# Kernel tuning notes

Hardware: AMD Instinct MI355X
Metric: run time of the kernel (lower is better)

## Reference

```python
import jax, jax.numpy as jnp
import numpy as np

B, S, D, H = 2, 2048, 1024, 16
DH = D // H  # 64


def setup_inputs() -> dict:
    key = jax.random.key(0)
    ks = jax.random.split(key, 12)
    std = 1.0 / np.sqrt(D)
    inp = {
        "query": jax.random.normal(ks[0], (B, S, D), jnp.float32),
        "key": jax.random.normal(ks[1], (B, S, D), jnp.float32),
        "value": jax.random.normal(ks[2], (B, S, D), jnp.float32),
        # causal mask: 1.0 where attention is disallowed (j > i)
        "mask": jnp.triu(jnp.ones((S, S), jnp.float32), k=1)[None, None, :, :] * jnp.ones((B, 1, 1, 1), jnp.float32),
        "Wq": jax.random.normal(ks[3], (D, D), jnp.float32) * std,
        "bq": jnp.zeros((D,), jnp.float32),
        "Wk": jax.random.normal(ks[4], (D, D), jnp.float32) * std,
        "bk": jnp.zeros((D,), jnp.float32),
        "Wv": jax.random.normal(ks[5], (D, D), jnp.float32) * std,
        "bv": jnp.zeros((D,), jnp.float32),
        "Wo": jax.random.normal(ks[6], (D, D), jnp.float32) * std,
        "bo": jnp.zeros((D,), jnp.float32),
    }
    return inp


def _split_heads(x):
    b, s, _ = x.shape
    return x.reshape(b, s, H, DH).transpose(0, 2, 1, 3)  # [B,H,S,DH]


def reference(query, key, value, mask, Wq, bq, Wk, bk, Wv, bv, Wo, bo):
    q = _split_heads(query @ Wq + bq)
    k = _split_heads(key @ Wk + bk)
    v = _split_heads(value @ Wv + bv)
    scale = jnp.sqrt(jnp.asarray(DH, jnp.float32))
    scores = jnp.einsum("bhqd,bhkd->bhqk", q, k) / scale
    scores = scores + mask * (-1e9)
    attn = jax.nn.softmax(scores, axis=-1)  # [B,H,S,S]
    out = jnp.einsum("bhqk,bhkd->bhqd", attn, v)
    out = out.transpose(0, 2, 1, 3).reshape(query.shape[0], -1, D)
    out = out @ Wo + bo
    return (out, attn)
```

## Files before the change

kernel.cpp:

```cpp
#include <hip/hip_runtime.h>
#include <hip/hip_bf16.h>

typedef __bf16 bf16;
typedef __bf16 bf16x8 __attribute__((ext_vector_type(8)));
typedef __bf16 bf16x4 __attribute__((ext_vector_type(4)));
typedef float f32x4 __attribute__((ext_vector_type(4)));

#define S_LEN 2048
#define D_MODEL 1024
#define N_HEADS 16
#define D_HEAD 64
#define M_ROWS 4096

__global__ void cvt_f32_bf16(const float* __restrict__ in, bf16* __restrict__ out, int n) {
    int i = (blockIdx.x * blockDim.x + threadIdx.x) * 4;
    int stride = gridDim.x * blockDim.x * 4;
    for (; i < n; i += stride) {
        f32x4 v = *(const f32x4*)(in + i);
        bf16x4 o;
        o[0] = (bf16)v[0]; o[1] = (bf16)v[1]; o[2] = (bf16)v[2]; o[3] = (bf16)v[3];
        *(bf16x4*)(out + i) = o;
    }
}

__global__ void cvtT_f32_bf16(const float* __restrict__ in, bf16* __restrict__ out) {
    __shared__ float t[32][33];
    int k0 = blockIdx.x * 32, n0 = blockIdx.y * 32;
    int lr = threadIdx.x & 31, lc = threadIdx.x >> 5;
#pragma unroll
    for (int p = 0; p < 4; ++p)
        t[lc + p * 8][lr] = in[(size_t)(k0 + lc + p * 8) * D_MODEL + n0 + lr];
    __syncthreads();
#pragma unroll
    for (int p = 0; p < 4; ++p)
        out[(size_t)(n0 + lc + p * 8) * D_MODEL + k0 + lr] = (bf16)t[lr][lc + p * 8];
}

__global__ __launch_bounds__(256) void gemm_bf16(
    const bf16* __restrict__ A, const bf16* __restrict__ Bt,
    const float* __restrict__ bias, bf16* __restrict__ outh,
    float* __restrict__ outf, int mode) {
    const int K = D_MODEL;
    __shared__ bf16 Als[128][80];
    __shared__ bf16 Bls[128][80];
    const int tid = threadIdx.x;
    const int lane = tid & 63, wave = tid >> 6;
    const int wm = wave >> 1, wn = wave & 1;
    const int g = lane >> 4, r16 = lane & 15;
    const int m0 = blockIdx.x * 128, n0 = blockIdx.y * 128;
    const int srow = tid >> 3, scol = (tid & 7) * 8;
    f32x4 acc[4][4] = {};
    for (int kt = 0; kt < K; kt += 64) {
        __syncthreads();
#pragma unroll
        for (int p = 0; p < 4; ++p) {
            int row = p * 32 + srow;
            *(bf16x8*)&Als[row][scol] = *(const bf16x8*)(A + (size_t)(m0 + row) * K + kt + scol);
            *(bf16x8*)&Bls[row][scol] = *(const bf16x8*)(Bt + (size_t)(n0 + row) * K + kt + scol);
        }
        __syncthreads();
#pragma unroll
        for (int kk = 0; kk < 2; ++kk) {
            bf16x8 af[4], bfr[4];
#pragma unroll
            for (int i = 0; i < 4; ++i) af[i] = *(const bf16x8*)&Als[wm * 64 + i * 16 + r16][kk * 32 + g * 8];
#pragma unroll
            for (int j = 0; j < 4; ++j) bfr[j] = *(const bf16x8*)&Bls[wn * 64 + j * 16 + r16][kk * 32 + g * 8];
#pragma unroll
            for (int i = 0; i < 4; ++i)
#pragma unroll
                for (int j = 0; j < 4; ++j)
                    acc[i][j] = __builtin_amdgcn_mfma_f32_16x16x32_bf16(af[i], bfr[j], acc[i][j], 0, 0, 0);
        }
    }
#pragma unroll
    for (int i = 0; i < 4; ++i) {
#pragma unroll
        for (int j = 0; j < 4; ++j) {
            int col = n0 + wn * 64 + j * 16 + r16;
            float bv = bias[col];
#pragma unroll
            for (int r = 0; r < 4; ++r) {
                int row = m0 + wm * 64 + i * 16 + g * 4 + r;
                float v = acc[i][j][r] + bv;
                if (mode == 0) {
                    int b = row >> 11, s = row & (S_LEN - 1);
                    int h = col >> 6, dh = col & 63;
                    outh[(size_t)(((b * N_HEADS + h) * S_LEN) + s) * D_HEAD + dh] = (bf16)v;
                } else if (mode == 1) {
                    outf[(size_t)row * D_MODEL + col] = v;
                } else {
                    int b = row >> 11, s = row & (S_LEN - 1);
                    int h = col >> 6, dh = col & 63;
                    outh[(((size_t)(b * N_HEADS + h)) * D_HEAD + dh) * S_LEN + s] = (bf16)v;
                }
            }
        }
    }
}

__global__ __launch_bounds__(256) void attn_fused(
    const bf16* __restrict__ Qh, const bf16* __restrict__ Kh, const bf16* __restrict__ VT,
    float* __restrict__ attn, bf16* __restrict__ ctx) {
    const int S = S_LEN, DH = D_HEAD;
    __shared__ bf16 Kls[64][80];
    __shared__ bf16 Vls[64][80];
    __shared__ bf16 Pls[4][16][80];
    __shared__ float rowinv[64];
    const int tid = threadIdx.x;
    const int lane = tid & 63, w = tid >> 6;
    const int g = lane >> 4, r16 = lane & 15;
    const int id = blockIdx.x;
    const int bh = id & 31;
    const int qx = id >> 5;
    const int a = qx & 7, kq = qx >> 3;
    const int qt = (kq == 0) ? (31 - a) : (kq == 1) ? (16 + a) : (kq == 2) ? (15 - a) : a;
    const int q0 = qt * 64;

    bf16x8 qa[2];
#pragma unroll
    for (int kk = 0; kk < 2; ++kk)
        qa[kk] = *(const bf16x8*)(Qh + (size_t)(bh * S + q0 + w * 16 + r16) * DH + kk * 32 + g * 8);

    float rs[4] = {0.f, 0.f, 0.f, 0.f};
    f32x4 oacc[4] = {};
    for (int kt = 0; kt <= qt; ++kt) {
        __syncthreads();
#pragma unroll
        for (int sIt = 0; sIt < 2; ++sIt) {
            int slot = tid + sIt * 256;
            int srow = slot >> 3, c8 = (slot & 7) * 8;
            *(bf16x8*)&Kls[srow][c8] =
                *(const bf16x8*)(Kh + (size_t)(bh * S + kt * 64 + srow) * DH + c8);
            *(bf16x8*)&Vls[srow][c8] =
                *(const bf16x8*)(VT + ((size_t)bh * DH + srow) * S + kt * 64 + c8);
        }
        __syncthreads();
#pragma unroll
        for (int n = 0; n < 4; ++n) {
            f32x4 s = {0.f, 0.f, 0.f, 0.f};
#pragma unroll
            for (int kk = 0; kk < 2; ++kk) {
                bf16x8 kb = *(const bf16x8*)&Kls[n * 16 + r16][kk * 32 + g * 8];
                s = __builtin_amdgcn_mfma_f32_16x16x32_bf16(qa[kk], kb, s, 0, 0, 0);
            }
            int col = kt * 64 + n * 16 + r16;
#pragma unroll
            for (int r = 0; r < 4; ++r) {
                int row = q0 + w * 16 + g * 4 + r;
                float p = (col <= row) ? __expf(s[r] * 0.125f) : 0.f;
                rs[r] += p;
                attn[(size_t)(bh * S + row) * S + col] = p;
                Pls[w][g * 4 + r][n * 16 + r16] = (bf16)p;
            }
        }
#pragma unroll
        for (int d = 0; d < 4; ++d) {
#pragma unroll
            for (int kk = 0; kk < 2; ++kk) {
                bf16x8 pa = *(const bf16x8*)&Pls[w][r16][kk * 32 + g * 8];
                bf16x8 vb = *(const bf16x8*)&Vls[d * 16 + r16][kk * 32 + g * 8];
                oacc[d] = __builtin_amdgcn_mfma_f32_16x16x32_bf16(pa, vb, oacc[d], 0, 0, 0);
            }
        }
    }
#pragma unroll
    for (int r = 0; r < 4; ++r) {
        rs[r] += __shfl_xor(rs[r], 1);
        rs[r] += __shfl_xor(rs[r], 2);
        rs[r] += __shfl_xor(rs[r], 4);
        rs[r] += __shfl_xor(rs[r], 8);
    }
    float inv[4];
#pragma unroll
    for (int r = 0; r < 4; ++r) inv[r] = 1.f / rs[r];
    if (r16 == 0) {
#pragma unroll
        for (int r = 0; r < 4; ++r) rowinv[w * 16 + g * 4 + r] = inv[r];
    }
    const int b = bh >> 4, h = bh & 15;
#pragma unroll
    for (int d = 0; d < 4; ++d) {
#pragma unroll
        for (int r = 0; r < 4; ++r) {
            int srowg = q0 + w * 16 + g * 4 + r;
            ctx[(size_t)(b * S + srowg) * D_MODEL + h * D_HEAD + d * 16 + r16] =
                (bf16)(oacc[d][r] * inv[r]);
        }
    }
    __syncthreads();
    {
        int rr = tid >> 2, q4 = (tid & 3) * 4;
        int row = q0 + rr;
        float sc = rowinv[rr];
        float* prow = attn + (size_t)(bh * S + row) * S;
        int limit = row + 1;
        for (int c = q4; c < S; c += 16) {
            if (c + 4 <= limit) {
                f32x4 v = *(f32x4*)(prow + c);
                v *= sc;
                *(f32x4*)(prow + c) = v;
            } else if (c >= limit) {
                f32x4 z = {0.f, 0.f, 0.f, 0.f};
                *(f32x4*)(prow + c) = z;
            } else {
#pragma unroll
                for (int e = 0; e < 4; ++e)
                    prow[c + e] = (c + e < limit) ? prow[c + e] * sc : 0.f;
            }
        }
    }
}

extern "C" void kernel_launch(void* const* d_in, const int* in_sizes, int n_in,
                              void* d_out, int out_size, void* d_ws, size_t ws_size,
                              hipStream_t stream) {
    const float* query = (const float*)d_in[0];
    const float* key   = (const float*)d_in[1];
    const float* value = (const float*)d_in[2];
    const float* Wq = (const float*)d_in[4];
    const float* bq = (const float*)d_in[5];
    const float* Wk = (const float*)d_in[6];
    const float* bk = (const float*)d_in[7];
    const float* Wv = (const float*)d_in[8];
    const float* bv = (const float*)d_in[9];
    const float* Wo = (const float*)d_in[10];
    const float* bo = (const float*)d_in[11];

    float* out  = (float*)d_out;
    float* attn = out + (size_t)M_ROWS * D_MODEL;

    bf16* ws  = (bf16*)d_ws;
    const size_t MD = (size_t)M_ROWS * D_MODEL;
    const size_t DD = (size_t)D_MODEL * D_MODEL;
    bf16* Xq  = ws;
    bf16* Xk  = Xq + MD;
    bf16* Xv  = Xk + MD;
    bf16* WqT = Xv + MD;
    bf16* WkT = WqT + DD;
    bf16* WvT = WkT + DD;
    bf16* WoT = WvT + DD;
    bf16* Qh  = WoT + DD;
    bf16* Kh  = Qh + MD;
    bf16* VT  = Kh + MD;
    bf16* Ctx = VT + MD;

    int n = (int)MD;
    cvt_f32_bf16<<<2048, 256, 0, stream>>>(query, Xq, n);
    cvt_f32_bf16<<<2048, 256, 0, stream>>>(key, Xk, n);
    cvt_f32_bf16<<<2048, 256, 0, stream>>>(value, Xv, n);
    dim3 tg(32, 32);
    cvtT_f32_bf16<<<tg, 256, 0, stream>>>(Wq, WqT);
    cvtT_f32_bf16<<<tg, 256, 0, stream>>>(Wk, WkT);
    cvtT_f32_bf16<<<tg, 256, 0, stream>>>(Wv, WvT);
    cvtT_f32_bf16<<<tg, 256, 0, stream>>>(Wo, WoT);

    dim3 gg(M_ROWS / 128, D_MODEL / 128);
    gemm_bf16<<<gg, 256, 0, stream>>>(Xq, WqT, bq, Qh, nullptr, 0);
    gemm_bf16<<<gg, 256, 0, stream>>>(Xk, WkT, bk, Kh, nullptr, 0);
    gemm_bf16<<<gg, 256, 0, stream>>>(Xv, WvT, bv, VT, nullptr, 2);

    attn_fused<<<1024, 256, 0, stream>>>(Qh, Kh, VT, attn, Ctx);

    gemm_bf16<<<gg, 256, 0, stream>>>(Ctx, WoT, bo, nullptr, out, 1);
}
```

Baseline: 946.1 us.

## Two-pass attention: precompute row sums, write normalized probabilities once, async GEMM loads

The attention kernel now makes a first pass over K tiles that only computes exp-score row sums. A second pass writes already-normalized probabilities directly to the attn output with vectorized stores, which removes the old read-modify-write rescale sweep over the whole attn row. QK is computed transposed so each lane holds four consecutive columns, which allows f32x4 stores, and the remaining tail past the diagonal is zero-filled. The GEMM staging switches to global_load_lds async copies into unpadded LDS tiles. The cost is recomputing QK^T twice, and the unpadded GEMM tiles may introduce LDS bank conflicts.

```diff
diff --git a/kernel.cpp b/kernel.cpp
--- a/kernel.cpp
+++ b/kernel.cpp
@@ -11,6 +11,12 @@
 #define N_HEADS 16
 #define D_HEAD 64
 #define M_ROWS 4096
+
+__device__ __forceinline__ void async_copy16(void* lds, const void* g) {
+    __builtin_amdgcn_global_load_lds(
+        (const __attribute__((address_space(1))) unsigned int*)g,
+        (__attribute__((address_space(3))) unsigned int*)lds, 16, 0, 0);
+}
 
 __global__ void cvt_f32_bf16(const float* __restrict__ in, bf16* __restrict__ out, int n) {
     int i = (blockIdx.x * blockDim.x + threadIdx.x) * 4;
@@ -41,22 +47,24 @@
     const float* __restrict__ bias, bf16* __restrict__ outh,
     float* __restrict__ outf, int mode) {
     const int K = D_MODEL;
-    __shared__ bf16 Als[128][80];
-    __shared__ bf16 Bls[128][80];
+    __shared__ bf16 Als[128][64];
+    __shared__ bf16 Bls[128][64];
     const int tid = threadIdx.x;
     const int lane = tid & 63, wave = tid >> 6;
     const int wm = wave >> 1, wn = wave & 1;
     const int g = lane >> 4, r16 = lane & 15;
     const int m0 = blockIdx.x * 128, n0 = blockIdx.y * 128;
-    const int srow = tid >> 3, scol = (tid & 7) * 8;
+    const int crow = lane >> 3;
+    const int ccol = (lane & 7) * 8;
     f32x4 acc[4][4] = {};
     for (int kt = 0; kt < K; kt += 64) {
         __syncthreads();
 #pragma unroll
-        for (int p = 0; p < 4; ++p) {
-            int row = p * 32 + srow;
-            *(bf16x8*)&Als[row][scol] = *(const bf16x8*)(A + (size_t)(m0 + row) * K + kt + scol);
-            *(bf16x8*)&Bls[row][scol] = *(const bf16x8*)(Bt + (size_t)(n0 + row) * K + kt + scol);
+        for (int i = 0; i < 4; ++i) {
+            int c = wave * 4 + i;
+            int row = c * 8 + crow;
+            async_copy16(&Als[c * 8][0], A + (size_t)(m0 + row) * K + kt + ccol);
+            async_copy16(&Bls[c * 8][0], Bt + (size_t)(n0 + row) * K + kt + ccol);
         }
         __syncthreads();
 #pragma unroll
@@ -105,7 +113,7 @@
     const int S = S_LEN, DH = D_HEAD;
     __shared__ bf16 Kls[64][80];
     __shared__ bf16 Vls[64][80];
-    __shared__ bf16 Pls[4][16][80];
+    __shared__ bf16 Pls[4][16][72];
     __shared__ float rowinv[64];
     const int tid = threadIdx.x;
     const int lane = tid & 63, w = tid >> 6;
@@ -116,13 +124,48 @@
     const int a = qx & 7, kq = qx >> 3;
     const int qt = (kq == 0) ? (31 - a) : (kq == 1) ? (16 + a) : (kq == 2) ? (15 - a) : a;
     const int q0 = qt * 64;
+    const int qrow = q0 + w * 16 + r16;
 
     bf16x8 qa[2];
 #pragma unroll
     for (int kk = 0; kk < 2; ++kk)
-        qa[kk] = *(const bf16x8*)(Qh + (size_t)(bh * S + q0 + w * 16 + r16) * DH + kk * 32 + g * 8);
-
-    float rs[4] = {0.f, 0.f, 0.f, 0.f};
+        qa[kk] = *(const bf16x8*)(Qh + (size_t)(bh * S + qrow) * DH + kk * 32 + g * 8);
+
+    float rs = 0.f;
+    for (int kt = 0; kt <= qt; ++kt) {
+        __syncthreads();
+#pragma unroll
+        for (int sIt = 0; sIt < 2; ++sIt) {
+            int slot = tid + sIt * 256;
+            int srow = slot >> 3, c8 = (slot & 7) * 8;
+            *(bf16x8*)&Kls[srow][c8] =
+                *(const bf16x8*)(Kh + (size_t)(bh * S + kt * 64 + srow) * DH + c8);
+        }
+        __syncthreads();
+#pragma unroll
+        for (int n = 0; n < 4; ++n) {
+            f32x4 s = {0.f, 0.f, 0.f, 0.f};
+#pragma unroll
+            for (int kk = 0; kk < 2; ++kk) {
+                bf16x8 kb = *(const bf16x8*)&Kls[n * 16 + r16][kk * 32 + g * 8];
+                s = __builtin_amdgcn_mfma_f32_16x16x32_bf16(kb, qa[kk], s, 0, 0, 0);
+            }
+            if (kt < qt) {
+#pragma unroll
+                for (int r = 0; r < 4; ++r) rs += __expf(s[r] * 0.125f);
+            } else {
+                int colb = kt * 64 + n * 16 + g * 4;
+#pragma unroll
+                for (int r = 0; r < 4; ++r)
+                    rs += (colb + r <= qrow) ? __expf(s[r] * 0.125f) : 0.f;
+            }
+        }
+    }
+    rs += __shfl_xor(rs, 16);
+    rs += __shfl_xor(rs, 32);
+    const float inv = 1.f / rs;
+    if (lane < 16) rowinv[w * 16 + lane] = inv;
+
     f32x4 oacc[4] = {};
     for (int kt = 0; kt <= qt; ++kt) {
         __syncthreads();
@@ -142,18 +185,26 @@
 #pragma unroll
             for (int kk = 0; kk < 2; ++kk) {
                 bf16x8 kb = *(const bf16x8*)&Kls[n * 16 + r16][kk * 32 + g * 8];
-                s = __builtin_amdgcn_mfma_f32_16x16x32_bf16(qa[kk], kb, s, 0, 0, 0);
-            }
-            int col = kt * 64 + n * 16 + r16;
-#pragma unroll
-            for (int r = 0; r < 4; ++r) {
-                int row = q0 + w * 16 + g * 4 + r;
-                float p = (col <= row) ? __expf(s[r] * 0.125f) : 0.f;
-                rs[r] += p;
-                attn[(size_t)(bh * S + row) * S + col] = p;
-                Pls[w][g * 4 + r][n * 16 + r16] = (bf16)p;
-            }
-        }
+                s = __builtin_amdgcn_mfma_f32_16x16x32_bf16(kb, qa[kk], s, 0, 0, 0);
+            }
+            int colb = kt * 64 + n * 16 + g * 4;
+            float p[4];
+            if (kt < qt) {
+#pragma unroll
+                for (int r = 0; r < 4; ++r) p[r] = __expf(s[r] * 0.125f);
+            } else {
+#pragma unroll
+                for (int r = 0; r < 4; ++r)
+                    p[r] = (colb + r <= qrow) ? __expf(s[r] * 0.125f) : 0.f;
+            }
+            f32x4 pw = {p[0] * inv, p[1] * inv, p[2] * inv, p[3] * inv};
+            *(f32x4*)(attn + (size_t)(bh * S + qrow) * S + colb) = pw;
+            bf16x4 pb;
+#pragma unroll
+            for (int r = 0; r < 4; ++r) pb[r] = (bf16)p[r];
+            *(bf16x4*)&Pls[w][r16][n * 16 + g * 4] = pb;
+        }
+        __syncthreads();
 #pragma unroll
         for (int d = 0; d < 4; ++d) {
 #pragma unroll
@@ -164,50 +215,26 @@
             }
         }
     }
-#pragma unroll
-    for (int r = 0; r < 4; ++r) {
-        rs[r] += __shfl_xor(rs[r], 1);
-        rs[r] += __shfl_xor(rs[r], 2);
-        rs[r] += __shfl_xor(rs[r], 4);
-        rs[r] += __shfl_xor(rs[r], 8);
-    }
-    float inv[4];
-#pragma unroll
-    for (int r = 0; r < 4; ++r) inv[r] = 1.f / rs[r];
-    if (r16 == 0) {
-#pragma unroll
-        for (int r = 0; r < 4; ++r) rowinv[w * 16 + g * 4 + r] = inv[r];
-    }
+    __syncthreads();
     const int b = bh >> 4, h = bh & 15;
+    float invr[4];
+#pragma unroll
+    for (int r = 0; r < 4; ++r) invr[r] = rowinv[w * 16 + g * 4 + r];
 #pragma unroll
     for (int d = 0; d < 4; ++d) {
 #pragma unroll
         for (int r = 0; r < 4; ++r) {
             int srowg = q0 + w * 16 + g * 4 + r;
             ctx[(size_t)(b * S + srowg) * D_MODEL + h * D_HEAD + d * 16 + r16] =
-                (bf16)(oacc[d][r] * inv[r]);
-        }
-    }
-    __syncthreads();
-    {
-        int rr = tid >> 2, q4 = (tid & 3) * 4;
-        int row = q0 + rr;
-        float sc = rowinv[rr];
-        float* prow = attn + (size_t)(bh * S + row) * S;
-        int limit = row + 1;
-        for (int c = q4; c < S; c += 16) {
-            if (c + 4 <= limit) {
-                f32x4 v = *(f32x4*)(prow + c);
-                v *= sc;
-                *(f32x4*)(prow + c) = v;
-            } else if (c >= limit) {
-                f32x4 z = {0.f, 0.f, 0.f, 0.f};
-                *(f32x4*)(prow + c) = z;
-            } else {
-#pragma unroll
-                for (int e = 0; e < 4; ++e)
-                    prow[c + e] = (c + e < limit) ? prow[c + e] * sc : 0.f;
-            }
+                (bf16)(oacc[d][r] * invr[r]);
+        }
+    }
+    int zstart = (qt + 1) * 64;
+    for (int rr = 0; rr < 64; ++rr) {
+        float* dst = attn + (size_t)(bh * S + q0 + rr) * S;
+        for (int c = zstart + tid * 4; c < S; c += 1024) {
+            f32x4 z = {0.f, 0.f, 0.f, 0.f};
+            *(f32x4*)(dst + c) = z;
         }
     }
 }
```

Measured after the change: 806.5 us. -14.8%, faster.
